# Kernel optimization log

Measured on AMD Instinct MI355X. Metric: run time of the kernel, lower is better.

Reference implementation:

```python
import jax, jax.numpy as jnp
import numpy as np

N, E, IN_C, HID, HEADS, OUT_C, NG = 50000, 800000, 300, 64, 2, 2, 256


def _lin(key, fan_in, fan_out):
    k1, k2 = jax.random.split(key)
    lim = 1.0 / np.sqrt(fan_in)
    W = jax.random.uniform(k1, (fan_in, fan_out), jnp.float32, -lim, lim)
    b = jax.random.uniform(k2, (fan_out,), jnp.float32, -lim, lim)
    return W, b


def setup_inputs() -> dict:
    key = jax.random.key(0)
    ks = jax.random.split(key, 16)
    x = jax.random.normal(ks[0], (N, IN_C), jnp.float32)
    edge_index = jax.random.randint(ks[1], (2, E), 0, N, jnp.int64)
    batch = jnp.sort(jax.random.randint(ks[2], (N,), 0, NG, jnp.int64))
    d = {"x": x, "edge_index": edge_index, "batch": batch}
    d["syn_W"], d["syn_b"] = _lin(ks[3], IN_C, HID)
    d["ant_W"], d["ant_b"] = _lin(ks[4], IN_C, HID)
    d["fus_W"], d["fus_b"] = _lin(ks[5], 2 * HID, HID * HEADS)
    # conv1: in=HID*HEADS, out=HID, heads=HEADS (concat)
    d["c1_Wq"], d["c1_bq"] = _lin(ks[6], HID * HEADS, HEADS * HID)
    d["c1_Wk"], d["c1_bk"] = _lin(ks[7], HID * HEADS, HEADS * HID)
    d["c1_Wv"], d["c1_bv"] = _lin(ks[8], HID * HEADS, HEADS * HID)
    d["c1_Ws"], d["c1_bs"] = _lin(ks[9], HID * HEADS, HEADS * HID)
    # conv2: in=HID*HEADS, out=HID, heads=1
    d["c2_Wq"], d["c2_bq"] = _lin(ks[10], HID * HEADS, HID)
    d["c2_Wk"], d["c2_bk"] = _lin(ks[11], HID * HEADS, HID)
    d["c2_Wv"], d["c2_bv"] = _lin(ks[12], HID * HEADS, HID)
    d["c2_Ws"], d["c2_bs"] = _lin(ks[13], HID * HEADS, HID)
    d["l1_W"], d["l1_b"] = _lin(ks[14], HID, HID)
    d["l2_W"], d["l2_b"] = _lin(ks[15], HID, OUT_C)
    return d


def transformer_conv(x, src, dst, Wq, bq, Wk, bk, Wv, bv, Ws, bs, heads, d_head):
    # PyG TransformerConv (concat=True, root_weight=True, eval mode)
    q = (x @ Wq + bq).reshape(-1, heads, d_head)  # [N,H,D]
    k = (x @ Wk + bk).reshape(-1, heads, d_head)
    v = (x @ Wv + bv).reshape(-1, heads, d_head)
    qi = q[dst]  # [E,H,D]
    kj = k[src]
    vj = v[src]
    alpha = jnp.einsum("ehd,ehd->eh", qi, kj) / jnp.sqrt(jnp.float32(d_head))
    amax = jax.ops.segment_max(alpha, dst, num_segments=x.shape[0])
    ealpha = jnp.exp(alpha - amax[dst])
    denom = jax.ops.segment_sum(ealpha, dst, num_segments=x.shape[0])
    alpha = ealpha / (denom[dst] + 1e-16)
    out = jax.ops.segment_sum(alpha[..., None] * vj, dst, num_segments=x.shape[0])
    out = out.reshape(x.shape[0], heads * d_head)
    return out + x @ Ws + bs


def reference(x, edge_index, batch, syn_W, syn_b, ant_W, ant_b, fus_W, fus_b,
              c1_Wq, c1_bq, c1_Wk, c1_bk, c1_Wv, c1_bv, c1_Ws, c1_bs,
              c2_Wq, c2_bq, c2_Wk, c2_bk, c2_Wv, c2_bv, c2_Ws, c2_bs,
              l1_W, l1_b, l2_W, l2_b):
    src, dst = edge_index[0], edge_index[1]
    x_syn = jax.nn.relu(x @ syn_W + syn_b)
    x_ant = jax.nn.relu(x @ ant_W + ant_b)
    x_fused = jnp.concatenate([x_syn, x_ant], axis=1) @ fus_W + fus_b  # [N, HID*HEADS]
    h = transformer_conv(x_fused, src, dst, c1_Wq, c1_bq, c1_Wk, c1_bk,
                         c1_Wv, c1_bv, c1_Ws, c1_bs, HEADS, HID)
    h = jax.nn.relu(h)
    h = transformer_conv(h, src, dst, c2_Wq, c2_bq, c2_Wk, c2_bk,
                         c2_Wv, c2_bv, c2_Ws, c2_bs, 1, HID)
    # global mean pool over graphs
    sums = jax.ops.segment_sum(h, batch, num_segments=NG)
    cnts = jax.ops.segment_sum(jnp.ones((h.shape[0], 1), h.dtype), batch, num_segments=NG)
    pooled = sums / jnp.maximum(cnts, 1.0)
    out = jax.nn.relu(pooled @ l1_W + l1_b)
    return out @ l2_W + l2_b
```

## Files before the change

kernel.cpp:

```cpp
#include <hip/hip_runtime.h>
#include <math.h>

#define NNODES 50000
#define NEDGES 800000
#define INC    300
#define NGRAPH 256

typedef __attribute__((ext_vector_type(8))) short bf16x8;
typedef __attribute__((ext_vector_type(4))) short bf16x4;
typedef __attribute__((ext_vector_type(4))) float f32x4;

#define L2E8 0.180336880f
#define SW(row, k) ((k) ^ (((row) & 7) << 3))
#define EB 3125
#define FRONT_BLOCKS 782

__device__ __forceinline__ unsigned short f2bf(float f) {
    unsigned u = __float_as_uint(f);
    u += 0x7fffu + ((u >> 16) & 1u);
    return (unsigned short)(u >> 16);
}
__device__ __forceinline__ float bf2f(unsigned short h) {
    return __uint_as_float(((unsigned)h) << 16);
}

struct WTArgs {
    const float* w[11];
    unsigned short* o[11];
    int K[11];
    int N[11];
    const float* syn_b; const float* ant_b;
    const float* c1q; const float* c1k; const float* c1v; const float* c1s;
    const float* c2q; const float* c2k; const float* c2v; const float* c2s;
    float* enc_b;
    float* c1_b;
    float* c2_b;
};

__global__ void k_setup(WTArgs a, const int* __restrict__ dstv, int* __restrict__ deg) {
    int bx = blockIdx.x;
    if (bx < EB) {
        int e = bx * 256 + threadIdx.x;
        if (e < NEDGES) atomicAdd(&deg[dstv[e]], 1);
        return;
    }
    bx -= EB;
    int which = bx / 75;
    int sub = bx - which * 75;
    if (which == 11) {
        if (sub != 0) return;
        int t = threadIdx.x;
        for (int u = t; u < 896; u += 256) {
            if (u < 512) {
                int s = u >> 7, r = u & 127;
                const float* p = (s == 0) ? a.c1q : (s == 1) ? a.c1k : (s == 2) ? a.c1v : a.c1s;
                a.c1_b[u] = p[r];
            } else if (u < 768) {
                int v = u - 512;
                int s = v >> 6, r = v & 63;
                const float* p = (s == 0) ? a.c2q : (s == 1) ? a.c2k : (s == 2) ? a.c2v : a.c2s;
                a.c2_b[v] = p[r];
            } else {
                int v = u - 768;
                a.enc_b[v] = (v < 64) ? a.syn_b[v] : a.ant_b[v - 64];
            }
        }
        return;
    }
    int i = sub * 256 + threadIdx.x;
    int K = a.K[which], N = a.N[which];
    if (i >= K * N) return;
    int k = i / N, n = i - k * N;
    a.o[which][(size_t)n * K + k] = f2bf(a.w[which][i]);
}

__global__ void k_scan1(const int* __restrict__ deg, int* __restrict__ ex,
                        int* __restrict__ bsum, int n) {
    __shared__ int tmp[256];
    int i = blockIdx.x * 256 + threadIdx.x;
    int v = (i < n) ? deg[i] : 0;
    tmp[threadIdx.x] = v;
    __syncthreads();
    for (int off = 1; off < 256; off <<= 1) {
        int t = (threadIdx.x >= off) ? tmp[threadIdx.x - off] : 0;
        __syncthreads();
        tmp[threadIdx.x] += t;
        __syncthreads();
    }
    if (i < n) ex[i] = tmp[threadIdx.x] - v;
    if (threadIdx.x == 255) bsum[blockIdx.x] = tmp[255];
}

__global__ void k_scan2(int* __restrict__ bsum, int nb) {
    __shared__ int tmp[256];
    int v = (threadIdx.x < nb) ? bsum[threadIdx.x] : 0;
    tmp[threadIdx.x] = v;
    __syncthreads();
    for (int off = 1; off < 256; off <<= 1) {
        int t = (threadIdx.x >= off) ? tmp[threadIdx.x - off] : 0;
        __syncthreads();
        tmp[threadIdx.x] += t;
        __syncthreads();
    }
    if (threadIdx.x < nb) bsum[threadIdx.x] = tmp[threadIdx.x] - v;
}

__global__ void k_scan3(int* __restrict__ rp, const int* __restrict__ bsum,
                        int* __restrict__ cursor, int n, int E) {
    int i = blockIdx.x * 256 + threadIdx.x;
    if (i < n) {
        int r = rp[i] + bsum[blockIdx.x];
        rp[i] = r;
        cursor[i] = r;
    }
    if (i == 0) rp[n] = E;
}

__global__ __launch_bounds__(256) void k_front_fill(
    const float* __restrict__ x,
    const unsigned short* __restrict__ enc_t, const float* __restrict__ enc_b,
    const unsigned short* __restrict__ fus_t, const float* __restrict__ fus_b,
    const unsigned short* __restrict__ c1w_t, const float* __restrict__ c1_b,
    unsigned short* __restrict__ qkvs1, int M,
    const int* __restrict__ src, const int* __restrict__ dstv,
    int* __restrict__ cursor, int* __restrict__ esrc)
{
    if (blockIdx.x >= FRONT_BLOCKS) {
        int e = (blockIdx.x - FRONT_BLOCKS) * 256 + threadIdx.x;
        if (e < NEDGES) {
            int d = dstv[e];
            int p = atomicAdd(&cursor[d], 1);
            esrc[p] = src[e];
        }
        return;
    }
    __shared__ __align__(16) short As[64 * 64];
    __shared__ __align__(16) short Bs[128 * 64];
    __shared__ __align__(16) short bufI[64 * 128];
    const int tid = threadIdx.x;
    const int bm = blockIdx.x * 64;
    const int tr = tid >> 4;
    const int tc = (tid & 15) * 4;
    const int l  = tid & 63;
    const int wv = tid >> 6;
    const int fr = l & 15;
    const int fg = l >> 4;

    f32x4 acc1[8];
    #pragma unroll
    for (int j = 0; j < 8; ++j) acc1[j] = (f32x4){0.f, 0.f, 0.f, 0.f};

    for (int k0 = 0; k0 < INC; k0 += 64) {
        #pragma unroll
        for (int p = 0; p < 4; ++p) {
            int row = p * 16 + tr;
            int grow = bm + row;
            int k = k0 + tc;
            float x0 = 0.f, x1 = 0.f, x2 = 0.f, x3 = 0.f;
            if (grow < M) {
                if (k + 4 <= INC) {
                    float4 a4 = *reinterpret_cast<const float4*>(x + (size_t)grow * INC + k);
                    x0 = a4.x; x1 = a4.y; x2 = a4.z; x3 = a4.w;
                } else {
                    if (k + 0 < INC) x0 = x[(size_t)grow * INC + k + 0];
                    if (k + 1 < INC) x1 = x[(size_t)grow * INC + k + 1];
                    if (k + 2 < INC) x2 = x[(size_t)grow * INC + k + 2];
                    if (k + 3 < INC) x3 = x[(size_t)grow * INC + k + 3];
                }
            }
            bf16x4 s4 = { (short)f2bf(x0), (short)f2bf(x1), (short)f2bf(x2), (short)f2bf(x3) };
            *reinterpret_cast<bf16x4*>(As + row * 64 + SW(row, tc)) = s4;
        }
        #pragma unroll
        for (int p = 0; p < 8; ++p) {
            int n = p * 16 + tr;
            int k = k0 + tc;
            bf16x4 s4;
            if (k + 4 <= INC) {
                s4 = *reinterpret_cast<const bf16x4*>(enc_t + (size_t)n * INC + k);
            } else {
                short e0 = 0, e1 = 0, e2 = 0, e3 = 0;
                if (k + 0 < INC) e0 = (short)enc_t[(size_t)n * INC + k + 0];
                if (k + 1 < INC) e1 = (short)enc_t[(size_t)n * INC + k + 1];
                if (k + 2 < INC) e2 = (short)enc_t[(size_t)n * INC + k + 2];
                if (k + 3 < INC) e3 = (short)enc_t[(size_t)n * INC + k + 3];
                s4 = (bf16x4){ e0, e1, e2, e3 };
            }
            *reinterpret_cast<bf16x4*>(Bs + n * 64 + SW(n, tc)) = s4;
        }
        __syncthreads();
        #pragma unroll
        for (int ks = 0; ks < 2; ++ks) {
            int kk = ks * 32 + fg * 8;
            int ar = wv * 16 + fr;
            bf16x8 a0 = *reinterpret_cast<const bf16x8*>(As + ar * 64 + SW(ar, kk));
            #pragma unroll
            for (int nj = 0; nj < 8; ++nj) {
                int br = nj * 16 + fr;
                bf16x8 b = *reinterpret_cast<const bf16x8*>(Bs + br * 64 + SW(br, kk));
                acc1[nj] = __builtin_amdgcn_mfma_f32_16x16x32_bf16(a0, b, acc1[nj], 0, 0, 0);
            }
        }
        __syncthreads();
    }
    #pragma unroll
    for (int nj = 0; nj < 8; ++nj) {
        int col = nj * 16 + fr;
        float bv = enc_b[col];
        #pragma unroll
        for (int r = 0; r < 4; ++r) {
            int row = wv * 16 + fg * 4 + r;
            float val = fmaxf(acc1[nj][r] + bv, 0.f);
            bufI[row * 128 + SW(row, col)] = (short)f2bf(val);
        }
    }
    __syncthreads();

    bf16x8 af[4];
    {
        int ar = wv * 16 + fr;
        #pragma unroll
        for (int t = 0; t < 4; ++t)
            af[t] = *reinterpret_cast<const bf16x8*>(bufI + ar * 128 + SW(ar, fg * 8 + t * 32));
    }

    f32x4 acc2[8];
    #pragma unroll
    for (int j = 0; j < 8; ++j) acc2[j] = (f32x4){0.f, 0.f, 0.f, 0.f};

    #pragma unroll
    for (int c = 0; c < 2; ++c) {
        __syncthreads();
        #pragma unroll
        for (int p = 0; p < 8; ++p) {
            int n = p * 16 + tr;
            *reinterpret_cast<bf16x4*>(Bs + n * 64 + SW(n, tc)) =
                *reinterpret_cast<const bf16x4*>(fus_t + (size_t)n * 128 + c * 64 + tc);
        }
        __syncthreads();
        #pragma unroll
        for (int ks = 0; ks < 2; ++ks) {
            int t = c * 2 + ks;
            int kk = ks * 32 + fg * 8;
            #pragma unroll
            for (int nj = 0; nj < 8; ++nj) {
                int br = nj * 16 + fr;
                bf16x8 b = *reinterpret_cast<const bf16x8*>(Bs + br * 64 + SW(br, kk));
                acc2[nj] = __builtin_amdgcn_mfma_f32_16x16x32_bf16(af[t], b, acc2[nj], 0, 0, 0);
            }
        }
    }
    __syncthreads();
    #pragma unroll
    for (int nj = 0; nj < 8; ++nj) {
        int col = nj * 16 + fr;
        float bv = fus_b[col];
        #pragma unroll
        for (int r = 0; r < 4; ++r) {
            int row = wv * 16 + fg * 4 + r;
            bufI[row * 128 + SW(row, col)] = (short)f2bf(acc2[nj][r] + bv);
        }
    }
    __syncthreads();

    bf16x8 af2[4];
    {
        int ar = wv * 16 + fr;
        #pragma unroll
        for (int t = 0; t < 4; ++t)
            af2[t] = *reinterpret_cast<const bf16x8*>(bufI + ar * 128 + SW(ar, fg * 8 + t * 32));
    }

    #pragma unroll
    for (int cc = 0; cc < 4; ++cc) {
        f32x4 acc3[8];
        #pragma unroll
        for (int j = 0; j < 8; ++j) acc3[j] = (f32x4){0.f, 0.f, 0.f, 0.f};
        #pragma unroll
        for (int c = 0; c < 2; ++c) {
            __syncthreads();
            #pragma unroll
            for (int p = 0; p < 8; ++p) {
                int n = p * 16 + tr;
                *reinterpret_cast<bf16x4*>(Bs + n * 64 + SW(n, tc)) =
                    *reinterpret_cast<const bf16x4*>(c1w_t + (size_t)(cc * 128 + n) * 128 + c * 64 + tc);
            }
            __syncthreads();
            #pragma unroll
            for (int ks = 0; ks < 2; ++ks) {
                int t = c * 2 + ks;
                int kk = ks * 32 + fg * 8;
                #pragma unroll
                for (int nj = 0; nj < 8; ++nj) {
                    int br = nj * 16 + fr;
                    bf16x8 b = *reinterpret_cast<const bf16x8*>(Bs + br * 64 + SW(br, kk));
                    acc3[nj] = __builtin_amdgcn_mfma_f32_16x16x32_bf16(af2[t], b, acc3[nj], 0, 0, 0);
                }
            }
        }
        #pragma unroll
        for (int nj = 0; nj < 8; ++nj) {
            int col = cc * 128 + nj * 16 + fr;
            float bv = c1_b[col];
            #pragma unroll
            for (int r = 0; r < 4; ++r) {
                int gr = bm + wv * 16 + fg * 4 + r;
                if (gr < M)
                    qkvs1[(size_t)gr * 512 + col] = f2bf(acc3[nj][r] + bv);
            }
        }
    }
}

#define BM 128

template<int BNT>
__global__ __launch_bounds__(256) void gemm_mfma(
    const unsigned short* __restrict__ A, int lda, int M, int K,
    const unsigned short* __restrict__ Wt,
    const float* __restrict__ bias,
    unsigned short* __restrict__ C, int ldc)
{
    __shared__ __align__(16) short As[BM * 64];
    __shared__ __align__(16) short Bs[BNT * 64];
    const int tid = threadIdx.x;
    const int bm = blockIdx.x * BM;
    const int bn = blockIdx.y * BNT;
    const int tr = tid >> 4;
    const int tc = (tid & 15) * 4;
    const int l  = tid & 63;
    const int wv = tid >> 6;
    const int fr = l & 15;
    const int fg = l >> 4;

    f32x4 acc[2][BNT / 16];
    #pragma unroll
    for (int i = 0; i < 2; ++i)
        #pragma unroll
        for (int j = 0; j < BNT / 16; ++j) acc[i][j] = (f32x4){0.f, 0.f, 0.f, 0.f};

    for (int k0 = 0; k0 < K; k0 += 64) {
        #pragma unroll
        for (int p = 0; p < 8; ++p) {
            int row = p * 16 + tr;
            int grow = bm + row;
            int k = k0 + tc;
            bf16x4 s4 = (bf16x4){0, 0, 0, 0};
            if (grow < M) s4 = *reinterpret_cast<const bf16x4*>(A + (size_t)grow * lda + k);
            *reinterpret_cast<bf16x4*>(As + row * 64 + SW(row, tc)) = s4;
        }
        #pragma unroll
        for (int p = 0; p < BNT / 16; ++p) {
            int n = p * 16 + tr;
            *reinterpret_cast<bf16x4*>(Bs + n * 64 + SW(n, tc)) =
                *reinterpret_cast<const bf16x4*>(Wt + (size_t)(bn + n) * K + k0 + tc);
        }
        __syncthreads();
        #pragma unroll
        for (int ks = 0; ks < 2; ++ks) {
            int kk = ks * 32 + fg * 8;
            int ar0 = wv * 32 + fr, ar1 = wv * 32 + 16 + fr;
            bf16x8 a0 = *reinterpret_cast<const bf16x8*>(As + ar0 * 64 + SW(ar0, kk));
            bf16x8 a1 = *reinterpret_cast<const bf16x8*>(As + ar1 * 64 + SW(ar1, kk));
            #pragma unroll
            for (int nj = 0; nj < BNT / 16; ++nj) {
                int br = nj * 16 + fr;
                bf16x8 b = *reinterpret_cast<const bf16x8*>(Bs + br * 64 + SW(br, kk));
                acc[0][nj] = __builtin_amdgcn_mfma_f32_16x16x32_bf16(a0, b, acc[0][nj], 0, 0, 0);
                acc[1][nj] = __builtin_amdgcn_mfma_f32_16x16x32_bf16(a1, b, acc[1][nj], 0, 0, 0);
            }
        }
        __syncthreads();
    }
    #pragma unroll
    for (int mi = 0; mi < 2; ++mi) {
        int row0 = bm + wv * 32 + mi * 16 + fg * 4;
        #pragma unroll
        for (int nj = 0; nj < BNT / 16; ++nj) {
            int col = bn + nj * 16 + fr;
            float bv = bias[col];
            #pragma unroll
            for (int r = 0; r < 4; ++r) {
                int gr = row0 + r;
                if (gr >= M) continue;
                C[(size_t)gr * ldc + col] = f2bf(acc[mi][nj][r] + bv);
            }
        }
    }
}

__global__ __launch_bounds__(256) void attn_h2(
    const unsigned short* __restrict__ qkvs,
    const int* __restrict__ rowptr, const int* __restrict__ esrc,
    unsigned short* __restrict__ outp, int N)
{
    int wid = (blockIdx.x * blockDim.x + threadIdx.x) >> 6;
    int l = threadIdx.x & 63;
    if (wid >= N) return;
    const int sl = l & 15;
    const int g  = l >> 4;
    const unsigned short* bi = qkvs + (size_t)wid * 512;
    float q[8];
    {
        bf16x8 qv = *reinterpret_cast<const bf16x8*>(bi + 8 * sl);
        #pragma unroll
        for (int i = 0; i < 8; ++i) q[i] = bf2f((unsigned short)qv[i]) * L2E8;
    }
    float s = 0.f;
    float acc[8] = {0.f, 0.f, 0.f, 0.f, 0.f, 0.f, 0.f, 0.f};
    const int beg = rowptr[wid], end = rowptr[wid + 1];
    const int iters = (end - beg + 3) >> 2;
    int e = beg + g;
    bool va0 = e < end;
    {
        int j = va0 ? esrc[e] : wid;
        const unsigned short* p0 = qkvs + (size_t)j * 512 + 8 * sl;
    }
    int j0 = va0 ? esrc[e] : wid;
    const unsigned short* pp0 = qkvs + (size_t)j0 * 512 + 8 * sl;
    bf16x8 ka = *reinterpret_cast<const bf16x8*>(pp0 + 128);
    bf16x8 vva = *reinterpret_cast<const bf16x8*>(pp0 + 256);
    bool va1 = (e + 4) < end;
    int j1 = va1 ? esrc[e + 4] : wid;
    const unsigned short* pp1 = qkvs + (size_t)j1 * 512 + 8 * sl;
    bf16x8 kb = *reinterpret_cast<const bf16x8*>(pp1 + 128);
    bf16x8 vvb = *reinterpret_cast<const bf16x8*>(pp1 + 256);
    for (int it = 0; it < iters; ++it) {
        bf16x8 kc = ka, vc = vva;
        bool vd = va0;
        ka = kb; vva = vvb; va0 = va1;
        va1 = (e + 8) < end;
        int j2 = va1 ? esrc[e + 8] : wid;
        const unsigned short* p2 = qkvs + (size_t)j2 * 512 + 8 * sl;
        kb = *reinterpret_cast<const bf16x8*>(p2 + 128);
        vvb = *reinterpret_cast<const bf16x8*>(p2 + 256);
        e += 4;
        float p = 0.f;
        #pragma unroll
        for (int i = 0; i < 8; ++i) p += q[i] * bf2f((unsigned short)kc[i]);
        p += __shfl_xor(p, 1, 64);
        p += __shfl_xor(p, 2, 64);
        p += __shfl_xor(p, 4, 64);
        float w = vd ? __builtin_amdgcn_exp2f(p) : 0.f;
        s += w;
        #pragma unroll
        for (int i = 0; i < 8; ++i) acc[i] += w * bf2f((unsigned short)vc[i]);
    }
    #pragma unroll
    for (int mask = 16; mask <= 32; mask <<= 1) {
        s += __shfl_xor(s, mask, 64);
        #pragma unroll
        for (int i = 0; i < 8; ++i) acc[i] += __shfl_xor(acc[i], mask, 64);
    }
    if (g == 0) {
        float inv = 1.f / (s + 1e-16f);
        bf16x8 sv = *reinterpret_cast<const bf16x8*>(bi + 384 + 8 * sl);
        bf16x8 o;
        #pragma unroll
        for (int i = 0; i < 8; ++i) {
            float r = fmaxf(acc[i] * inv + bf2f((unsigned short)sv[i]), 0.f);
            o[i] = (short)f2bf(r);
        }
        *reinterpret_cast<bf16x8*>(outp + (size_t)wid * 128 + 8 * sl) = o;
    }
}

__global__ __launch_bounds__(256) void attn_h1(
    const unsigned short* __restrict__ qkvs,
    const int* __restrict__ rowptr, const int* __restrict__ esrc,
    float* __restrict__ outp, int N)
{
    int wid = (blockIdx.x * blockDim.x + threadIdx.x) >> 6;
    int l = threadIdx.x & 63;
    if (wid >= N) return;
    const int sl = l & 7;
    const int g  = l >> 3;
    const unsigned short* bi = qkvs + (size_t)wid * 256;
    float q[8];
    {
        bf16x8 qv = *reinterpret_cast<const bf16x8*>(bi + 8 * sl);
        #pragma unroll
        for (int i = 0; i < 8; ++i) q[i] = bf2f((unsigned short)qv[i]) * L2E8;
    }
    float s = 0.f;
    float acc[8] = {0.f, 0.f, 0.f, 0.f, 0.f, 0.f, 0.f, 0.f};
    const int beg = rowptr[wid], end = rowptr[wid + 1];
    const int iters = (end - beg + 7) >> 3;
    int e = beg + g;
    bool va0 = e < end;
    int j0 = va0 ? esrc[e] : wid;
    const unsigned short* pp0 = qkvs + (size_t)j0 * 256 + 8 * sl;
    bf16x8 ka = *reinterpret_cast<const bf16x8*>(pp0 + 64);
    bf16x8 vva = *reinterpret_cast<const bf16x8*>(pp0 + 128);
    bool va1 = (e + 8) < end;
    int j1 = va1 ? esrc[e + 8] : wid;
    const unsigned short* pp1 = qkvs + (size_t)j1 * 256 + 8 * sl;
    bf16x8 kb = *reinterpret_cast<const bf16x8*>(pp1 + 64);
    bf16x8 vvb = *reinterpret_cast<const bf16x8*>(pp1 + 128);
    for (int it = 0; it < iters; ++it) {
        bf16x8 kc = ka, vc = vva;
        bool vd = va0;
        ka = kb; vva = vvb; va0 = va1;
        va1 = (e + 16) < end;
        int j2 = va1 ? esrc[e + 16] : wid;
        const unsigned short* p2 = qkvs + (size_t)j2 * 256 + 8 * sl;
        kb = *reinterpret_cast<const bf16x8*>(p2 + 64);
        vvb = *reinterpret_cast<const bf16x8*>(p2 + 128);
        e += 8;
        float p = 0.f;
        #pragma unroll
        for (int i = 0; i < 8; ++i) p += q[i] * bf2f((unsigned short)kc[i]);
        p += __shfl_xor(p, 1, 64);
        p += __shfl_xor(p, 2, 64);
        p += __shfl_xor(p, 4, 64);
        float w = vd ? __builtin_amdgcn_exp2f(p) : 0.f;
        s += w;
        #pragma unroll
        for (int i = 0; i < 8; ++i) acc[i] += w * bf2f((unsigned short)vc[i]);
    }
    #pragma unroll
    for (int mask = 8; mask <= 32; mask <<= 1) {
        s += __shfl_xor(s, mask, 64);
        #pragma unroll
        for (int i = 0; i < 8; ++i) acc[i] += __shfl_xor(acc[i], mask, 64);
    }
    if (g == 0) {
        float inv = 1.f / (s + 1e-16f);
        float r[8];
        #pragma unroll
        for (int i = 0; i < 8; ++i)
            r[i] = acc[i] * inv + bf2f(bi[192 + 8 * sl + i]);
        float* op = outp + (size_t)wid * 64 + 8 * sl;
        *reinterpret_cast<float4*>(op)     = make_float4(r[0], r[1], r[2], r[3]);
        *reinterpret_cast<float4*>(op + 4) = make_float4(r[4], r[5], r[6], r[7]);
    }
}

__device__ __forceinline__ int lbound(const int* __restrict__ a, int n, int key) {
    int lo = 0, hi = n;
    while (lo < hi) {
        int mid = (lo + hi) >> 1;
        if (a[mid] < key) lo = mid + 1; else hi = mid;
    }
    return lo;
}

__global__ void pool_head(const float* __restrict__ h, const int* __restrict__ batch,
                          const float* __restrict__ l1W, const float* __restrict__ l1b,
                          const float* __restrict__ l2W, const float* __restrict__ l2b,
                          float* __restrict__ out) {
    __shared__ float red[4][64];
    int g = blockIdx.x;
    int l = threadIdx.x & 63;
    int w = threadIdx.x >> 6;
    int lo = lbound(batch, NNODES, g);
    int hi = lbound(batch, NNODES, g + 1);
    float s = 0.f;
    for (int i = lo + w; i < hi; i += 4) s += h[(size_t)i * 64 + l];
    red[w][l] = s;
    __syncthreads();
    if (w == 0) {
        float t = red[0][l] + red[1][l] + red[2][l] + red[3][l];
        float cnt = (float)((hi - lo) > 1 ? (hi - lo) : 1);
        float p = t / cnt;
        float hsum = l1b[l];
        #pragma unroll
        for (int kk = 0; kk < 64; ++kk) {
            float pk = __shfl(p, kk, 64);
            hsum += pk * l1W[kk * 64 + l];
        }
        float hr = fmaxf(hsum, 0.f);
        float o0 = hr * l2W[l * 2 + 0];
        float o1 = hr * l2W[l * 2 + 1];
        #pragma unroll
        for (int off = 32; off > 0; off >>= 1) {
            o0 += __shfl_xor(o0, off, 64);
            o1 += __shfl_xor(o1, off, 64);
        }
        if (l == 0) {
            out[g * 2 + 0] = o0 + l2b[0];
            out[g * 2 + 1] = o1 + l2b[1];
        }
    }
}

extern "C" void kernel_launch(void* const* d_in, const int* in_sizes, int n_in,
                              void* d_out, int out_size, void* d_ws, size_t ws_size,
                              hipStream_t stream) {
    const float* x      = (const float*)d_in[0];
    const int*   ei     = (const int*)d_in[1];
    const int*   batch  = (const int*)d_in[2];
    const float* syn_W  = (const float*)d_in[3];  const float* syn_b = (const float*)d_in[4];
    const float* ant_W  = (const float*)d_in[5];  const float* ant_b = (const float*)d_in[6];
    const float* fus_W  = (const float*)d_in[7];  const float* fus_b = (const float*)d_in[8];
    const float* c1_Wq  = (const float*)d_in[9];  const float* c1_bq = (const float*)d_in[10];
    const float* c1_Wk  = (const float*)d_in[11]; const float* c1_bk = (const float*)d_in[12];
    const float* c1_Wv  = (const float*)d_in[13]; const float* c1_bv = (const float*)d_in[14];
    const float* c1_Ws  = (const float*)d_in[15]; const float* c1_bs = (const float*)d_in[16];
    const float* c2_Wq  = (const float*)d_in[17]; const float* c2_bq = (const float*)d_in[18];
    const float* c2_Wk  = (const float*)d_in[19]; const float* c2_bk = (const float*)d_in[20];
    const float* c2_Wv  = (const float*)d_in[21]; const float* c2_bv = (const float*)d_in[22];
    const float* c2_Ws  = (const float*)d_in[23]; const float* c2_bs = (const float*)d_in[24];
    const float* l1_W   = (const float*)d_in[25]; const float* l1_b  = (const float*)d_in[26];
    const float* l2_W   = (const float*)d_in[27]; const float* l2_b  = (const float*)d_in[28];
    const int* src = ei;
    const int* dst = ei + NEDGES;
    float* out = (float*)d_out;

    char* ws = (char*)d_ws;
    size_t off = 0;
    auto alloc = [&](size_t bytes) -> char* {
        char* p = ws + off;
        off += (bytes + 255) & ~((size_t)255);
        return p;
    };

    unsigned short* H     = (unsigned short*)alloc((size_t)NNODES * 128 * 2);
    unsigned short* H2b   = (unsigned short*)alloc((size_t)NNODES * 128 * 2);
    unsigned short* qkvs1 = (unsigned short*)alloc((size_t)NNODES * 512 * 2);
    unsigned short* qkvs2 = (unsigned short*)alloc((size_t)NNODES * 256 * 2);
    unsigned short* enc_t = (unsigned short*)alloc((size_t)128 * 300 * 2);
    unsigned short* fus_t = (unsigned short*)alloc((size_t)128 * 128 * 2);
    unsigned short* c1w_t = (unsigned short*)alloc((size_t)512 * 128 * 2);
    unsigned short* c2w_t = (unsigned short*)alloc((size_t)256 * 128 * 2);
    float* enc_b = (float*)alloc(128 * 4);
    float* c1_b  = (float*)alloc(512 * 4);
    float* c2_b  = (float*)alloc(256 * 4);
    int*   deg    = (int*)alloc((NNODES + 1) * 4);
    int*   cursor = (int*)alloc((NNODES + 1) * 4);
    int*   rowptr = (int*)alloc((NNODES + 1) * 4);
    int*   bsum   = (int*)alloc(256 * 4);
    int*   esrc   = (int*)alloc((size_t)NEDGES * 4);

    const int NB = (NNODES + 255) / 256;
    dim3 t256(256);

    WTArgs wa;
    wa.w[0] = syn_W;  wa.o[0] = enc_t;             wa.K[0] = 300; wa.N[0] = 64;
    wa.w[1] = ant_W;  wa.o[1] = enc_t + 64 * 300;  wa.K[1] = 300; wa.N[1] = 64;
    wa.w[2] = fus_W;  wa.o[2] = fus_t;             wa.K[2] = 128; wa.N[2] = 128;
    wa.w[3] = c1_Wq;  wa.o[3] = c1w_t + 0 * 128 * 128; wa.K[3] = 128; wa.N[3] = 128;
    wa.w[4] = c1_Wk;  wa.o[4] = c1w_t + 1 * 128 * 128; wa.K[4] = 128; wa.N[4] = 128;
    wa.w[5] = c1_Wv;  wa.o[5] = c1w_t + 2 * 128 * 128; wa.K[5] = 128; wa.N[5] = 128;
    wa.w[6] = c1_Ws;  wa.o[6] = c1w_t + 3 * 128 * 128; wa.K[6] = 128; wa.N[6] = 128;
    wa.w[7] = c2_Wq;  wa.o[7] = c2w_t + 0 * 64 * 128;  wa.K[7] = 128; wa.N[7] = 64;
    wa.w[8] = c2_Wk;  wa.o[8] = c2w_t + 1 * 64 * 128;  wa.K[8] = 128; wa.N[8] = 64;
    wa.w[9] = c2_Wv;  wa.o[9] = c2w_t + 2 * 64 * 128;  wa.K[9] = 128; wa.N[9] = 64;
    wa.w[10] = c2_Ws; wa.o[10] = c2w_t + 3 * 64 * 128; wa.K[10] = 128; wa.N[10] = 64;
    wa.syn_b = syn_b; wa.ant_b = ant_b;
    wa.c1q = c1_bq; wa.c1k = c1_bk; wa.c1v = c1_bv; wa.c1s = c1_bs;
    wa.c2q = c2_bq; wa.c2k = c2_bk; wa.c2v = c2_bv; wa.c2s = c2_bs;
    wa.enc_b = enc_b; wa.c1_b = c1_b; wa.c2_b = c2_b;

    hipMemsetAsync(deg, 0, (NNODES + 1) * sizeof(int), stream);
    k_setup<<<EB + 900, t256, 0, stream>>>(wa, dst, deg);

    k_scan1<<<NB, t256, 0, stream>>>(deg, rowptr, bsum, NNODES);
    k_scan2<<<1, t256, 0, stream>>>(bsum, NB);
    k_scan3<<<NB, t256, 0, stream>>>(rowptr, bsum, cursor, NNODES, NEDGES);

    k_front_fill<<<FRONT_BLOCKS + EB, t256, 0, stream>>>(
        x, enc_t, enc_b, fus_t, fus_b, c1w_t, c1_b, qkvs1, NNODES,
        src, dst, cursor, esrc);

    attn_h2<<<(NNODES * 64 + 255) / 256, t256, 0, stream>>>(qkvs1, rowptr, esrc, H, NNODES);

    gemm_mfma<128><<<dim3((NNODES + BM - 1) / BM, 2), t256, 0, stream>>>(
        H, 128, NNODES, 128, c2w_t, c2_b, qkvs2, 256);

    float* H2 = (float*)H2b;
    attn_h1<<<(NNODES * 64 + 255) / 256, t256, 0, stream>>>(qkvs2, rowptr, esrc, H2, NNODES);

    pool_head<<<NGRAPH, t256, 0, stream>>>(H2, batch, l1_W, l1_b, l2_W, l2_b, out);
}
```

Baseline: 289.3 us.

## Pre-swizzle weight images for direct LDS copy and interleave front/fill blocks

Weights are written during setup in the exact swizzled, K-chunked LDS layout, so the front GEMM kernel fills shared memory with contiguous 16-byte copies instead of strided transposed loads with tail guards. Full 128-wide K tiles for the fusion and conv1 weights halve the number of barrier-separated chunks. Block indices are interleaved so every fifth block is a GEMM block and the rest do CSR fill, mixing compute-heavy and atomic-heavy work across CUs. This adds a memset of the encoder image and raises shared memory per block to 48KB, which may lower occupancy.

Result: no change. 286.3 us (-1.0%).

```diff
diff --git a/kernel.cpp b/kernel.cpp
--- a/kernel.cpp
+++ b/kernel.cpp
@@ -14,6 +14,7 @@
 #define SW(row, k) ((k) ^ (((row) & 7) << 3))
 #define EB 3125
 #define FRONT_BLOCKS 782
+#define FF_GRID (FRONT_BLOCKS + EB)
 
 __device__ __forceinline__ unsigned short f2bf(float f) {
     unsigned u = __float_as_uint(f);
@@ -29,6 +30,8 @@
     unsigned short* o[11];
     int K[11];
     int N[11];
+    int mode[11];
+    int roff[11];
     const float* syn_b; const float* ant_b;
     const float* c1q; const float* c1k; const float* c1v; const float* c1s;
     const float* c2q; const float* c2k; const float* c2v; const float* c2s;
@@ -71,7 +74,18 @@
     int K = a.K[which], N = a.N[which];
     if (i >= K * N) return;
     int k = i / N, n = i - k * N;
-    a.o[which][(size_t)n * K + k] = f2bf(a.w[which][i]);
+    unsigned short v = f2bf(a.w[which][i]);
+    size_t dst;
+    int m = a.mode[which];
+    if (m == 1) {
+        int row = a.roff[which] + n;
+        dst = (size_t)(k >> 6) * 8192 + row * 64 + SW(row, k & 63);
+    } else if (m == 2) {
+        dst = (size_t)n * 128 + SW(n, k);
+    } else {
+        dst = (size_t)n * K + k;
+    }
+    a.o[which][dst] = v;
 }
 
 __global__ void k_scan1(const int* __restrict__ deg, int* __restrict__ ex,
@@ -118,15 +132,20 @@
 
 __global__ __launch_bounds__(256) void k_front_fill(
     const float* __restrict__ x,
-    const unsigned short* __restrict__ enc_t, const float* __restrict__ enc_b,
-    const unsigned short* __restrict__ fus_t, const float* __restrict__ fus_b,
-    const unsigned short* __restrict__ c1w_t, const float* __restrict__ c1_b,
+    const unsigned short* __restrict__ enc_img, const float* __restrict__ enc_b,
+    const unsigned short* __restrict__ fus_img, const float* __restrict__ fus_b,
+    const unsigned short* __restrict__ c1_img, const float* __restrict__ c1_b,
     unsigned short* __restrict__ qkvs1, int M,
     const int* __restrict__ src, const int* __restrict__ dstv,
     int* __restrict__ cursor, int* __restrict__ esrc)
 {
-    if (blockIdx.x >= FRONT_BLOCKS) {
-        int e = (blockIdx.x - FRONT_BLOCKS) * 256 + threadIdx.x;
+    const int b = blockIdx.x;
+    const int q = b / 5, r5 = b - q * 5;
+    const int tid = threadIdx.x;
+    if (!(r5 == 0 && q < FRONT_BLOCKS)) {
+        int nf = (b + 4) / 5;
+        if (nf > FRONT_BLOCKS) nf = FRONT_BLOCKS;
+        int e = (b - nf) * 256 + tid;
         if (e < NEDGES) {
             int d = dstv[e];
             int p = atomicAdd(&cursor[d], 1);
@@ -134,11 +153,11 @@
         }
         return;
     }
-    __shared__ __align__(16) short As[64 * 64];
-    __shared__ __align__(16) short Bs[128 * 64];
-    __shared__ __align__(16) short bufI[64 * 128];
-    const int tid = threadIdx.x;
-    const int bm = blockIdx.x * 64;
+    __shared__ __align__(16) char pool[49152];
+    short* bufI = (short*)pool;
+    short* Bt   = (short*)(pool + 16384);
+    short* At   = (short*)(pool + 32768);
+    const int bm = q * 64;
     const int tr = tid >> 4;
     const int tc = (tid & 15) * 4;
     const int l  = tid & 63;
@@ -150,7 +169,14 @@
     #pragma unroll
     for (int j = 0; j < 8; ++j) acc1[j] = (f32x4){0.f, 0.f, 0.f, 0.f};
 
-    for (int k0 = 0; k0 < INC; k0 += 64) {
+    for (int ph = 0; ph < 5; ++ph) {
+        int k0 = ph * 64;
+        {
+            bf16x8* d = (bf16x8*)Bt;
+            const bf16x8* s = (const bf16x8*)(enc_img + ph * 8192);
+            #pragma unroll
+            for (int i = 0; i < 4; ++i) d[tid + i * 256] = s[tid + i * 256];
+        }
         #pragma unroll
         for (int p = 0; p < 4; ++p) {
             int row = p * 16 + tr;
@@ -169,36 +195,19 @@
                 }
             }
             bf16x4 s4 = { (short)f2bf(x0), (short)f2bf(x1), (short)f2bf(x2), (short)f2bf(x3) };
-            *reinterpret_cast<bf16x4*>(As + row * 64 + SW(row, tc)) = s4;
-        }
-        #pragma unroll
-        for (int p = 0; p < 8; ++p) {
-            int n = p * 16 + tr;
-            int k = k0 + tc;
-            bf16x4 s4;
-            if (k + 4 <= INC) {
-                s4 = *reinterpret_cast<const bf16x4*>(enc_t + (size_t)n * INC + k);
-            } else {
-                short e0 = 0, e1 = 0, e2 = 0, e3 = 0;
-                if (k + 0 < INC) e0 = (short)enc_t[(size_t)n * INC + k + 0];
-                if (k + 1 < INC) e1 = (short)enc_t[(size_t)n * INC + k + 1];
-                if (k + 2 < INC) e2 = (short)enc_t[(size_t)n * INC + k + 2];
-                if (k + 3 < INC) e3 = (short)enc_t[(size_t)n * INC + k + 3];
-                s4 = (bf16x4){ e0, e1, e2, e3 };
-            }
-            *reinterpret_cast<bf16x4*>(Bs + n * 64 + SW(n, tc)) = s4;
+            *reinterpret_cast<bf16x4*>(At + row * 64 + SW(row, tc)) = s4;
         }
         __syncthreads();
         #pragma unroll
         for (int ks = 0; ks < 2; ++ks) {
             int kk = ks * 32 + fg * 8;
             int ar = wv * 16 + fr;
-            bf16x8 a0 = *reinterpret_cast<const bf16x8*>(As + ar * 64 + SW(ar, kk));
+            bf16x8 a0 = *reinterpret_cast<const bf16x8*>(At + ar * 64 + SW(ar, kk));
             #pragma unroll
             for (int nj = 0; nj < 8; ++nj) {
                 int br = nj * 16 + fr;
-                bf16x8 b = *reinterpret_cast<const bf16x8*>(Bs + br * 64 + SW(br, kk));
-                acc1[nj] = __builtin_amdgcn_mfma_f32_16x16x32_bf16(a0, b, acc1[nj], 0, 0, 0);
+                bf16x8 bfr = *reinterpret_cast<const bf16x8*>(Bt + br * 64 + SW(br, kk));
+                acc1[nj] = __builtin_amdgcn_mfma_f32_16x16x32_bf16(a0, bfr, acc1[nj], 0, 0, 0);
             }
         }
         __syncthreads();
@@ -223,79 +232,70 @@
         for (int t = 0; t < 4; ++t)
             af[t] = *reinterpret_cast<const bf16x8*>(bufI + ar * 128 + SW(ar, fg * 8 + t * 32));
     }
+    __syncthreads();
+    {
+        bf16x8* d = (bf16x8*)Bt;
+        const bf16x8* s = (const bf16x8*)fus_img;
+        #pragma unroll
+        for (int i = 0; i < 8; ++i) d[tid + i * 256] = s[tid + i * 256];
+    }
+    __syncthreads();
 
     f32x4 acc2[8];
     #pragma unroll
     for (int j = 0; j < 8; ++j) acc2[j] = (f32x4){0.f, 0.f, 0.f, 0.f};
-
-    #pragma unroll
-    for (int c = 0; c < 2; ++c) {
-        __syncthreads();
-        #pragma unroll
-        for (int p = 0; p < 8; ++p) {
-            int n = p * 16 + tr;
-            *reinterpret_cast<bf16x4*>(Bs + n * 64 + SW(n, tc)) =
-                *reinterpret_cast<const bf16x4*>(fus_t + (size_t)n * 128 + c * 64 + tc);
-        }
-        __syncthreads();
-        #pragma unroll
-        for (int ks = 0; ks < 2; ++ks) {
-            int t = c * 2 + ks;
-            int kk = ks * 32 + fg * 8;
+    #pragma unroll
+    for (int t = 0; t < 4; ++t) {
+        int k = t * 32 + fg * 8;
+        #pragma unroll
+        for (int nj = 0; nj < 8; ++nj) {
+            int br = nj * 16 + fr;
+            bf16x8 bfr = *reinterpret_cast<const bf16x8*>(Bt + br * 128 + SW(br, k));
+            acc2[nj] = __builtin_amdgcn_mfma_f32_16x16x32_bf16(af[t], bfr, acc2[nj], 0, 0, 0);
+        }
+    }
+    __syncthreads();
+    #pragma unroll
+    for (int nj = 0; nj < 8; ++nj) {
+        int col = nj * 16 + fr;
+        float bv = fus_b[col];
+        #pragma unroll
+        for (int r = 0; r < 4; ++r) {
+            int row = wv * 16 + fg * 4 + r;
+            bufI[row * 128 + SW(row, col)] = (short)f2bf(acc2[nj][r] + bv);
+        }
+    }
+    __syncthreads();
+
+    bf16x8 af2[4];
+    {
+        int ar = wv * 16 + fr;
+        #pragma unroll
+        for (int t = 0; t < 4; ++t)
+            af2[t] = *reinterpret_cast<const bf16x8*>(bufI + ar * 128 + SW(ar, fg * 8 + t * 32));
+    }
+
+    #pragma unroll
+    for (int cc = 0; cc < 4; ++cc) {
+        __syncthreads();
+        {
+            bf16x8* d = (bf16x8*)Bt;
+            const bf16x8* s = (const bf16x8*)(c1_img + cc * 16384);
+            #pragma unroll
+            for (int i = 0; i < 8; ++i) d[tid + i * 256] = s[tid + i * 256];
+        }
+        __syncthreads();
+        f32x4 acc3[8];
+        #pragma unroll
+        for (int j = 0; j < 8; ++j) acc3[j] = (f32x4){0.f, 0.f, 0.f, 0.f};
+        #pragma unroll
+        for (int t = 0; t < 4; ++t) {
+            int k = t * 32 + fg * 8;
             #pragma unroll
             for (int nj = 0; nj < 8; ++nj) {
                 int br = nj * 16 + fr;
-                bf16x8 b = *reinterpret_cast<const bf16x8*>(Bs + br * 64 + SW(br, kk));
-                acc2[nj] = __builtin_amdgcn_mfma_f32_16x16x32_bf16(af[t], b, acc2[nj], 0, 0, 0);
-            }
-        }
-    }
-    __syncthreads();
-    #pragma unroll
-    for (int nj = 0; nj < 8; ++nj) {
-        int col = nj * 16 + fr;
-        float bv = fus_b[col];
-        #pragma unroll
-        for (int r = 0; r < 4; ++r) {
-            int row = wv * 16 + fg * 4 + r;
-            bufI[row * 128 + SW(row, col)] = (short)f2bf(acc2[nj][r] + bv);
-        }
-    }
-    __syncthreads();
-
-    bf16x8 af2[4];
-    {
-        int ar = wv * 16 + fr;
-        #pragma unroll
-        for (int t = 0; t < 4; ++t)
-            af2[t] = *reinterpret_cast<const bf16x8*>(bufI + ar * 128 + SW(ar, fg * 8 + t * 32));
-    }
-
-    #pragma unroll
-    for (int cc = 0; cc < 4; ++cc) {
-        f32x4 acc3[8];
-        #pragma unroll
-        for (int j = 0; j < 8; ++j) acc3[j] = (f32x4){0.f, 0.f, 0.f, 0.f};
-        #pragma unroll
-        for (int c = 0; c < 2; ++c) {
-            __syncthreads();
-            #pragma unroll
-            for (int p = 0; p < 8; ++p) {
-                int n = p * 16 + tr;
-                *reinterpret_cast<bf16x4*>(Bs + n * 64 + SW(n, tc)) =
-                    *reinterpret_cast<const bf16x4*>(c1w_t + (size_t)(cc * 128 + n) * 128 + c * 64 + tc);
-            }
-            __syncthreads();
-            #pragma unroll
-            for (int ks = 0; ks < 2; ++ks) {
-                int t = c * 2 + ks;
-                int kk = ks * 32 + fg * 8;
-                #pragma unroll
-                for (int nj = 0; nj < 8; ++nj) {
-                    int br = nj * 16 + fr;
-                    bf16x8 b = *reinterpret_cast<const bf16x8*>(Bs + br * 64 + SW(br, kk));
-                    acc3[nj] = __builtin_amdgcn_mfma_f32_16x16x32_bf16(af2[t], b, acc3[nj], 0, 0, 0);
-                }
+                bf16x8 bfr = *reinterpret_cast<const bf16x8*>(Bt + br * 128 + SW(br, k));
+                acc3[nj] = __builtin_amdgcn_mfma_f32_16x16x32_bf16(af2[t], bfr, acc3[nj], 0, 0, 0);
             }
         }
         #pragma unroll
@@ -412,10 +412,6 @@
     const int iters = (end - beg + 3) >> 2;
     int e = beg + g;
     bool va0 = e < end;
-    {
-        int j = va0 ? esrc[e] : wid;
-        const unsigned short* p0 = qkvs + (size_t)j * 512 + 8 * sl;
-    }
     int j0 = va0 ? esrc[e] : wid;
     const unsigned short* pp0 = qkvs + (size_t)j0 * 512 + 8 * sl;
     bf16x8 ka = *reinterpret_cast<const bf16x8*>(pp0 + 128);
@@ -619,10 +615,10 @@
     unsigned short* H2b   = (unsigned short*)alloc((size_t)NNODES * 128 * 2);
     unsigned short* qkvs1 = (unsigned short*)alloc((size_t)NNODES * 512 * 2);
     unsigned short* qkvs2 = (unsigned short*)alloc((size_t)NNODES * 256 * 2);
-    unsigned short* enc_t = (unsigned short*)alloc((size_t)128 * 300 * 2);
-    unsigned short* fus_t = (unsigned short*)alloc((size_t)128 * 128 * 2);
-    unsigned short* c1w_t = (unsigned short*)alloc((size_t)512 * 128 * 2);
-    unsigned short* c2w_t = (unsigned short*)alloc((size_t)256 * 128 * 2);
+    unsigned short* enc_img = (unsigned short*)alloc((size_t)5 * 8192 * 2);
+    unsigned short* fus_img = (unsigned short*)alloc((size_t)16384 * 2);
+    unsigned short* c1_img  = (unsigned short*)alloc((size_t)4 * 16384 * 2);
+    unsigned short* c2w_t   = (unsigned short*)alloc((size_t)256 * 128 * 2);
     float* enc_b = (float*)alloc(128 * 4);
     float* c1_b  = (float*)alloc(512 * 4);
     float* c2_b  = (float*)alloc(256 * 4);
@@ -636,31 +632,32 @@
     dim3 t256(256);
 
     WTArgs wa;
-    wa.w[0] = syn_W;  wa.o[0] = enc_t;             wa.K[0] = 300; wa.N[0] = 64;
-    wa.w[1] = ant_W;  wa.o[1] = enc_t + 64 * 300;  wa.K[1] = 300; wa.N[1] = 64;
-    wa.w[2] = fus_W;  wa.o[2] = fus_t;             wa.K[2] = 128; wa.N[2] = 128;
-    wa.w[3] = c1_Wq;  wa.o[3] = c1w_t + 0 * 128 * 128; wa.K[3] = 128; wa.N[3] = 128;
-    wa.w[4] = c1_Wk;  wa.o[4] = c1w_t + 1 * 128 * 128; wa.K[4] = 128; wa.N[4] = 128;
-    wa.w[5] = c1_Wv;  wa.o[5] = c1w_t + 2 * 128 * 128; wa.K[5] = 128; wa.N[5] = 128;
-    wa.w[6] = c1_Ws;  wa.o[6] = c1w_t + 3 * 128 * 128; wa.K[6] = 128; wa.N[6] = 128;
-    wa.w[7] = c2_Wq;  wa.o[7] = c2w_t + 0 * 64 * 128;  wa.K[7] = 128; wa.N[7] = 64;
-    wa.w[8] = c2_Wk;  wa.o[8] = c2w_t + 1 * 64 * 128;  wa.K[8] = 128; wa.N[8] = 64;
-    wa.w[9] = c2_Wv;  wa.o[9] = c2w_t + 2 * 64 * 128;  wa.K[9] = 128; wa.N[9] = 64;
-    wa.w[10] = c2_Ws; wa.o[10] = c2w_t + 3 * 64 * 128; wa.K[10] = 128; wa.N[10] = 64;
+    wa.w[0] = syn_W;  wa.o[0] = enc_img;  wa.K[0] = 300; wa.N[0] = 64;  wa.mode[0] = 1; wa.roff[0] = 0;
+    wa.w[1] = ant_W;  wa.o[1] = enc_img;  wa.K[1] = 300; wa.N[1] = 64;  wa.mode[1] = 1; wa.roff[1] = 64;
+    wa.w[2] = fus_W;  wa.o[2] = fus_img;  wa.K[2] = 128; wa.N[2] = 128; wa.mode[2] = 2; wa.roff[2] = 0;
+    wa.w[3] = c1_Wq;  wa.o[3] = c1_img + 0 * 16384; wa.K[3] = 128; wa.N[3] = 128; wa.mode[3] = 2; wa.roff[3] = 0;
+    wa.w[4] = c1_Wk;  wa.o[4] = c1_img + 1 * 16384; wa.K[4] = 128; wa.N[4] = 128; wa.mode[4] = 2; wa.roff[4] = 0;
+    wa.w[5] = c1_Wv;  wa.o[5] = c1_img + 2 * 16384; wa.K[5] = 128; wa.N[5] = 128; wa.mode[5] = 2; wa.roff[5] = 0;
+    wa.w[6] = c1_Ws;  wa.o[6] = c1_img + 3 * 16384; wa.K[6] = 128; wa.N[6] = 128; wa.mode[6] = 2; wa.roff[6] = 0;
+    wa.w[7] = c2_Wq;  wa.o[7] = c2w_t + 0 * 64 * 128;  wa.K[7] = 128; wa.N[7] = 64; wa.mode[7] = 0; wa.roff[7] = 0;
+    wa.w[8] = c2_Wk;  wa.o[8] = c2w_t + 1 * 64 * 128;  wa.K[8] = 128; wa.N[8] = 64; wa.mode[8] = 0; wa.roff[8] = 0;
+    wa.w[9] = c2_Wv;  wa.o[9] = c2w_t + 2 * 64 * 128;  wa.K[9] = 128; wa.N[9] = 64; wa.mode[9] = 0; wa.roff[9] = 0;
+    wa.w[10] = c2_Ws; wa.o[10] = c2w_t + 3 * 64 * 128; wa.K[10] = 128; wa.N[10] = 64; wa.mode[10] = 0; wa.roff[10] = 0;
     wa.syn_b = syn_b; wa.ant_b = ant_b;
     wa.c1q = c1_bq; wa.c1k = c1_bk; wa.c1v = c1_bv; wa.c1s = c1_bs;
     wa.c2q = c2_bq; wa.c2k = c2_bk; wa.c2v = c2_bv; wa.c2s = c2_bs;
     wa.enc_b = enc_b; wa.c1_b = c1_b; wa.c2_b = c2_b;
 
     hipMemsetAsync(deg, 0, (NNODES + 1) * sizeof(int), stream);
+    hipMemsetAsync(enc_img, 0, (size_t)5 * 8192 * 2, stream);
     k_setup<<<EB + 900, t256, 0, stream>>>(wa, dst, deg);
 
     k_scan1<<<NB, t256, 0, stream>>>(deg, rowptr, bsum, NNODES);
     k_scan2<<<1, t256, 0, stream>>>(bsum, NB);
     k_scan3<<<NB, t256, 0, stream>>>(rowptr, bsum, cursor, NNODES, NEDGES);
 
-    k_front_fill<<<FRONT_BLOCKS + EB, t256, 0, stream>>>(
-        x, enc_t, enc_b, fus_t, fus_b, c1w_t, c1_b, qkvs1, NNODES,
+    k_front_fill<<<FF_GRID, t256, 0, stream>>>(
+        x, enc_img, enc_b, fus_img, fus_b, c1_img, c1_b, qkvs1, NNODES,
         src, dst, cursor, esrc);
 
     attn_h2<<<(NNODES * 64 + 255) / 256, t256, 0, stream>>>(qkvs1, rowptr, esrc, H, NNODES);
```
